# Kernel tuning notes

Measured on AMD Instinct MI355X. Metric: run time of the kernel, lower is better.

The kernel has to match this reference:

```python
import jax, jax.numpy as jnp
import numpy as np

NEG = -1000.0  # fill value for unmatched (type_mask != ti) entries

B, N, R = 4, 48, 16
T = 2 * R + 1          # 33 transition channels
Nc, L = 80, 3          # chains, chain length
Nt, Ni = 16, 5         # triples, chains per triple (uniform c_sections)


def setup_inputs() -> dict:
    key = jax.random.key(0)
    k1, k2, k3, k4, k5 = jax.random.split(key, 5)
    transitions = jax.random.normal(k1, (B, N, N, T), dtype=jnp.float32)
    type_mask = jax.random.randint(k2, (B, N, N, R), 0, 2, dtype=jnp.int32)
    rules = jax.random.randint(k3, (Nc, L), 0, T, dtype=jnp.int32)
    # stacked per-triple weights [Nt, Ni] (orig: ParameterList of [Ni,1]) and biases [Nt]
    weights = jax.random.normal(k4, (Nt, Ni), dtype=jnp.float32) / np.sqrt(Ni)
    biases = jax.random.uniform(k5, (Nt,), dtype=jnp.float32, minval=-1.0, maxval=1.0)
    return {"transitions": transitions, "type_mask": type_mask, "rules": rules,
            "weights": weights, "biases": biases}


def path_scores(transitions, rules):
    """Tropical (max-plus) chain DP.
    transitions: [B,N,N,T], rules: [Nc,L] -> scores [B,N,N,Nc]
    scores[b,x,y,c] = max over intermediate nodes of sum of hop scores.
    """
    Lc = rules.shape[1]
    hops = [transitions[..., rules[:, l]] for l in range(Lc)]  # each [B,N,N,Nc]
    # max-plus "matmul": s[b,x,y,c] = max_k hops0[b,x,k,c] + hops1[b,k,y,c]
    s = jnp.max(hops[0][:, :, :, None, :] + hops[1][:, None, :, :, :], axis=2)
    for l in range(2, Lc):
        s = jnp.max(s[:, :, :, None, :] + hops[l][:, None, :, :, :], axis=2)
    return s


def reference(transitions, type_mask, rules, weights, biases):
    # scores over all chains, exponentiated: [B,N,N,Nc]
    s = jnp.exp(path_scores(transitions, rules))
    # group chains by triple (uniform sections): [B,N,N,Nt,Ni]
    s = s.reshape(s.shape[0], s.shape[1], s.shape[2], Nt, Ni)
    # per-triple weighted sum + bias; one triple per relation so Nt == R
    comb = jnp.einsum('bxytc,tc->bxyt', s, weights) + biases  # [B,N,N,R]
    # masked_scatter: write score where type_mask[...,i] == ti (== 0 here), else -1000
    out = jnp.where(type_mask == 0, comb, NEG)
    return out
```

## Files before the change

kernel.cpp:

```cpp
#include <hip/hip_runtime.h>
#include <cmath>

#define BB 4
#define NN 48
#define PP (NN * NN)
#define TT 33
#define RR 16
#define NC 80
#define NI 5
#define NEG (-1000.0f)

#define XH 24
#define RS 52

__global__ __launch_bounds__(256) void transpose_kernel(
    const float* __restrict__ trans,
    float*       __restrict__ tpose)
{
    __shared__ float tile[64 * TT];
    const int blk = blockIdx.x;
    const int b   = blk / 36;
    const int p0  = (blk - b * 36) * 64;

    const float4* src = (const float4*)(trans + ((size_t)b * PP + p0) * TT);
    for (int j = threadIdx.x; j < 64 * TT / 4; j += 256)
        ((float4*)tile)[j] = src[j];
    __syncthreads();

    for (int j = threadIdx.x; j < TT * 64; j += 256) {
        const int t  = j >> 6;
        const int pl = j & 63;
        tpose[((size_t)b * TT + t) * PP + p0 + pl] = tile[pl * TT + t];
    }
}

__global__ __launch_bounds__(192) void chain_dp_kernel(
    const float* __restrict__ tpose,
    const int*   __restrict__ rules,
    const float* __restrict__ weights,
    float*       __restrict__ sw)
{
    __shared__ float H0R[XH * RS];
    __shared__ float H1 [PP];
    __shared__ float H2 [PP];
    __shared__ float S1R[XH * RS];

    const int blk = blockIdx.x;
    const int bc  = blk >> 1;
    const int xh  = blk & 1;
    const int b   = bc / NC;
    const int c   = bc - b * NC;
    const int x0r = xh * XH;

    const int r0 = rules[c * 3 + 0];
    const int r1 = rules[c * 3 + 1];
    const int r2 = rules[c * 3 + 2];

    const float* p0 = tpose + ((size_t)b * TT + r0) * PP + (size_t)x0r * NN;
    const float* p1 = tpose + ((size_t)b * TT + r1) * PP;
    const float* p2 = tpose + ((size_t)b * TT + r2) * PP;

    for (int j = threadIdx.x; j < PP / 4; j += 192) {
        ((float4*)H1)[j] = ((const float4*)p1)[j];
        ((float4*)H2)[j] = ((const float4*)p2)[j];
    }
    for (int j = threadIdx.x; j < XH * NN / 4; j += 192) {
        const int row = j / 12;
        const int cw  = j - row * 12;
        *(float4*)&H0R[row * RS + cw * 4] = ((const float4*)p0)[j];
    }
    __syncthreads();

    const int yt = threadIdx.x % 24;
    const int xt = threadIdx.x / 24;
    const int x0 = xt * 3;
    const int y0 = yt * 2;

    float acc[3][2];
    #pragma unroll
    for (int jx = 0; jx < 3; ++jx) { acc[jx][0] = -INFINITY; acc[jx][1] = -INFINITY; }

    #pragma unroll 4
    for (int k4 = 0; k4 < NN; k4 += 4) {
        const float4 a0 = *(const float4*)&H0R[(x0 + 0) * RS + k4];
        const float4 a1 = *(const float4*)&H0R[(x0 + 1) * RS + k4];
        const float4 a2 = *(const float4*)&H0R[(x0 + 2) * RS + k4];
        const float2 b0 = *(const float2*)&H1[(k4 + 0) * NN + y0];
        const float2 b1 = *(const float2*)&H1[(k4 + 1) * NN + y0];
        const float2 b2 = *(const float2*)&H1[(k4 + 2) * NN + y0];
        const float2 b3 = *(const float2*)&H1[(k4 + 3) * NN + y0];
        const float av[3][4] = {{a0.x, a0.y, a0.z, a0.w},
                                {a1.x, a1.y, a1.z, a1.w},
                                {a2.x, a2.y, a2.z, a2.w}};
        const float bv[4][2] = {{b0.x, b0.y}, {b1.x, b1.y},
                                {b2.x, b2.y}, {b3.x, b3.y}};
        #pragma unroll
        for (int jx = 0; jx < 3; ++jx)
            #pragma unroll
            for (int jy = 0; jy < 2; ++jy) {
                const float s0 = av[jx][0] + bv[0][jy];
                const float s1 = av[jx][1] + bv[1][jy];
                const float s2 = av[jx][2] + bv[2][jy];
                const float s3 = av[jx][3] + bv[3][jy];
                acc[jx][jy] = fmaxf(acc[jx][jy], fmaxf(s0, s1));
                acc[jx][jy] = fmaxf(acc[jx][jy], fmaxf(s2, s3));
            }
    }

    #pragma unroll
    for (int jx = 0; jx < 3; ++jx) {
        float2 v; v.x = acc[jx][0]; v.y = acc[jx][1];
        *(float2*)&S1R[(x0 + jx) * RS + y0] = v;
    }
    __syncthreads();

    float acc2[3][2];
    #pragma unroll
    for (int jx = 0; jx < 3; ++jx) { acc2[jx][0] = -INFINITY; acc2[jx][1] = -INFINITY; }

    #pragma unroll 4
    for (int k4 = 0; k4 < NN; k4 += 4) {
        const float4 a0 = *(const float4*)&S1R[(x0 + 0) * RS + k4];
        const float4 a1 = *(const float4*)&S1R[(x0 + 1) * RS + k4];
        const float4 a2 = *(const float4*)&S1R[(x0 + 2) * RS + k4];
        const float2 b0 = *(const float2*)&H2[(k4 + 0) * NN + y0];
        const float2 b1 = *(const float2*)&H2[(k4 + 1) * NN + y0];
        const float2 b2 = *(const float2*)&H2[(k4 + 2) * NN + y0];
        const float2 b3 = *(const float2*)&H2[(k4 + 3) * NN + y0];
        const float av[3][4] = {{a0.x, a0.y, a0.z, a0.w},
                                {a1.x, a1.y, a1.z, a1.w},
                                {a2.x, a2.y, a2.z, a2.w}};
        const float bv[4][2] = {{b0.x, b0.y}, {b1.x, b1.y},
                                {b2.x, b2.y}, {b3.x, b3.y}};
        #pragma unroll
        for (int jx = 0; jx < 3; ++jx)
            #pragma unroll
            for (int jy = 0; jy < 2; ++jy) {
                const float s0 = av[jx][0] + bv[0][jy];
                const float s1 = av[jx][1] + bv[1][jy];
                const float s2 = av[jx][2] + bv[2][jy];
                const float s3 = av[jx][3] + bv[3][jy];
                acc2[jx][jy] = fmaxf(acc2[jx][jy], fmaxf(s0, s1));
                acc2[jx][jy] = fmaxf(acc2[jx][jy], fmaxf(s2, s3));
            }
    }

    const float wgt = weights[c];
    float* outp = sw + (size_t)bc * PP + (size_t)x0r * NN;
    #pragma unroll
    for (int jx = 0; jx < 3; ++jx) {
        float2 o;
        o.x = __expf(acc2[jx][0]) * wgt;
        o.y = __expf(acc2[jx][1]) * wgt;
        *(float2*)&outp[(x0 + jx) * NN + y0] = o;
    }
}

__global__ __launch_bounds__(256) void combine_kernel(
    const float* __restrict__ sw,
    const int*   __restrict__ mask,
    const float* __restrict__ biases,
    float*       __restrict__ out)
{
    const int tq = threadIdx.x >> 7;
    const int pl = blockIdx.x * 128 + (threadIdx.x & 127);
    if (pl >= BB * PP) return;
    const int b = pl / PP;
    const int p = pl - b * PP;

    const float* base = sw + (size_t)b * NC * PP + p;

    float acc[8];
    #pragma unroll
    for (int tt = 0; tt < 8; ++tt) {
        const int t = tq * 8 + tt;
        float s = biases[t];
        #pragma unroll
        for (int i = 0; i < NI; ++i)
            s += base[(size_t)(t * NI + i) * PP];
        acc[tt] = s;
    }

    const int4* m4 = (const int4*)(mask + (size_t)pl * RR + tq * 8);
    float4*     o4 = (float4*)(out + (size_t)pl * RR + tq * 8);
    #pragma unroll
    for (int q = 0; q < 2; ++q) {
        const int4 m = m4[q];
        float4 o;
        o.x = (m.x == 0) ? acc[q * 4 + 0] : NEG;
        o.y = (m.y == 0) ? acc[q * 4 + 1] : NEG;
        o.z = (m.z == 0) ? acc[q * 4 + 2] : NEG;
        o.w = (m.w == 0) ? acc[q * 4 + 3] : NEG;
        o4[q] = o;
    }
}

extern "C" void kernel_launch(void* const* d_in, const int* in_sizes, int n_in,
                              void* d_out, int out_size, void* d_ws, size_t ws_size,
                              hipStream_t stream)
{
    const float* trans   = (const float*)d_in[0];
    const int*   mask    = (const int*)  d_in[1];
    const int*   rules   = (const int*)  d_in[2];
    const float* weights = (const float*)d_in[3];
    const float* biases  = (const float*)d_in[4];
    float* out = (float*)d_out;

    float* tpose = (float*)d_ws;
    float* sw    = tpose + (size_t)BB * TT * PP;

    transpose_kernel<<<BB * 36, 256, 0, stream>>>(trans, tpose);

    chain_dp_kernel<<<BB * NC * 2, 192, 0, stream>>>(tpose, rules, weights, sw);

    const int total2 = BB * PP * 2;
    combine_kernel<<<(total2 + 255) / 256, 256, 0, stream>>>(sw, mask, biases, out);
}
```

Baseline: 75.04 us.

## Process full 48x48 tile per block instead of splitting rows across two blocks

Each block of the chain DP kernel now computes all 48 rows for one (batch, chain) pair instead of half. This avoids loading H1 and H2 twice, once per half-block, and each thread's micro-tile grows from 3x2 to 3x4 with float4 B-operand loads. The grid is halved to 320 blocks, which may reduce occupancy and parallelism across CUs. Shared memory per block also rises because the H0R and S1R buffers double.

New measurement: 75.22 us. No clear change (+0.2%).

```diff
diff --git a/kernel.cpp b/kernel.cpp
--- a/kernel.cpp
+++ b/kernel.cpp
@@ -10,7 +10,6 @@
 #define NI 5
 #define NEG (-1000.0f)
 
-#define XH 24
 #define RS 52
 
 __global__ __launch_bounds__(256) void transpose_kernel(
@@ -40,64 +39,64 @@
     const float* __restrict__ weights,
     float*       __restrict__ sw)
 {
-    __shared__ float H0R[XH * RS];
+    __shared__ float H0R[NN * RS];
     __shared__ float H1 [PP];
     __shared__ float H2 [PP];
-    __shared__ float S1R[XH * RS];
-
-    const int blk = blockIdx.x;
-    const int bc  = blk >> 1;
-    const int xh  = blk & 1;
-    const int b   = bc / NC;
-    const int c   = bc - b * NC;
-    const int x0r = xh * XH;
+    __shared__ float S1R[NN * RS];
+
+    const int bc = blockIdx.x;
+    const int b  = bc / NC;
+    const int c  = bc - b * NC;
 
     const int r0 = rules[c * 3 + 0];
     const int r1 = rules[c * 3 + 1];
     const int r2 = rules[c * 3 + 2];
 
-    const float* p0 = tpose + ((size_t)b * TT + r0) * PP + (size_t)x0r * NN;
+    const float* p0 = tpose + ((size_t)b * TT + r0) * PP;
     const float* p1 = tpose + ((size_t)b * TT + r1) * PP;
     const float* p2 = tpose + ((size_t)b * TT + r2) * PP;
 
+    #pragma unroll
     for (int j = threadIdx.x; j < PP / 4; j += 192) {
         ((float4*)H1)[j] = ((const float4*)p1)[j];
         ((float4*)H2)[j] = ((const float4*)p2)[j];
-    }
-    for (int j = threadIdx.x; j < XH * NN / 4; j += 192) {
         const int row = j / 12;
         const int cw  = j - row * 12;
         *(float4*)&H0R[row * RS + cw * 4] = ((const float4*)p0)[j];
     }
     __syncthreads();
 
-    const int yt = threadIdx.x % 24;
-    const int xt = threadIdx.x / 24;
+    const int yt = threadIdx.x % 12;
+    const int xt = threadIdx.x / 12;
     const int x0 = xt * 3;
-    const int y0 = yt * 2;
-
-    float acc[3][2];
-    #pragma unroll
-    for (int jx = 0; jx < 3; ++jx) { acc[jx][0] = -INFINITY; acc[jx][1] = -INFINITY; }
+    const int y0 = yt * 4;
+
+    float acc[3][4];
+    #pragma unroll
+    for (int jx = 0; jx < 3; ++jx)
+        #pragma unroll
+        for (int jy = 0; jy < 4; ++jy) acc[jx][jy] = -INFINITY;
 
     #pragma unroll 4
     for (int k4 = 0; k4 < NN; k4 += 4) {
         const float4 a0 = *(const float4*)&H0R[(x0 + 0) * RS + k4];
         const float4 a1 = *(const float4*)&H0R[(x0 + 1) * RS + k4];
         const float4 a2 = *(const float4*)&H0R[(x0 + 2) * RS + k4];
-        const float2 b0 = *(const float2*)&H1[(k4 + 0) * NN + y0];
-        const float2 b1 = *(const float2*)&H1[(k4 + 1) * NN + y0];
-        const float2 b2 = *(const float2*)&H1[(k4 + 2) * NN + y0];
-        const float2 b3 = *(const float2*)&H1[(k4 + 3) * NN + y0];
+        const float4 b0 = *(const float4*)&H1[(k4 + 0) * NN + y0];
+        const float4 b1 = *(const float4*)&H1[(k4 + 1) * NN + y0];
+        const float4 b2 = *(const float4*)&H1[(k4 + 2) * NN + y0];
+        const float4 b3 = *(const float4*)&H1[(k4 + 3) * NN + y0];
         const float av[3][4] = {{a0.x, a0.y, a0.z, a0.w},
                                 {a1.x, a1.y, a1.z, a1.w},
                                 {a2.x, a2.y, a2.z, a2.w}};
-        const float bv[4][2] = {{b0.x, b0.y}, {b1.x, b1.y},
-                                {b2.x, b2.y}, {b3.x, b3.y}};
+        const float bv[4][4] = {{b0.x, b0.y, b0.z, b0.w},
+                                {b1.x, b1.y, b1.z, b1.w},
+                                {b2.x, b2.y, b2.z, b2.w},
+                                {b3.x, b3.y, b3.z, b3.w}};
         #pragma unroll
         for (int jx = 0; jx < 3; ++jx)
             #pragma unroll
-            for (int jy = 0; jy < 2; ++jy) {
+            for (int jy = 0; jy < 4; ++jy) {
                 const float s0 = av[jx][0] + bv[0][jy];
                 const float s1 = av[jx][1] + bv[1][jy];
                 const float s2 = av[jx][2] + bv[2][jy];
@@ -109,33 +108,38 @@
 
     #pragma unroll
     for (int jx = 0; jx < 3; ++jx) {
-        float2 v; v.x = acc[jx][0]; v.y = acc[jx][1];
-        *(float2*)&S1R[(x0 + jx) * RS + y0] = v;
+        float4 v;
+        v.x = acc[jx][0]; v.y = acc[jx][1]; v.z = acc[jx][2]; v.w = acc[jx][3];
+        *(float4*)&S1R[(x0 + jx) * RS + y0] = v;
     }
     __syncthreads();
 
-    float acc2[3][2];
-    #pragma unroll
-    for (int jx = 0; jx < 3; ++jx) { acc2[jx][0] = -INFINITY; acc2[jx][1] = -INFINITY; }
+    float acc2[3][4];
+    #pragma unroll
+    for (int jx = 0; jx < 3; ++jx)
+        #pragma unroll
+        for (int jy = 0; jy < 4; ++jy) acc2[jx][jy] = -INFINITY;
 
     #pragma unroll 4
     for (int k4 = 0; k4 < NN; k4 += 4) {
         const float4 a0 = *(const float4*)&S1R[(x0 + 0) * RS + k4];
         const float4 a1 = *(const float4*)&S1R[(x0 + 1) * RS + k4];
         const float4 a2 = *(const float4*)&S1R[(x0 + 2) * RS + k4];
-        const float2 b0 = *(const float2*)&H2[(k4 + 0) * NN + y0];
-        const float2 b1 = *(const float2*)&H2[(k4 + 1) * NN + y0];
-        const float2 b2 = *(const float2*)&H2[(k4 + 2) * NN + y0];
-        const float2 b3 = *(const float2*)&H2[(k4 + 3) * NN + y0];
+        const float4 b0 = *(const float4*)&H2[(k4 + 0) * NN + y0];
+        const float4 b1 = *(const float4*)&H2[(k4 + 1) * NN + y0];
+        const float4 b2 = *(const float4*)&H2[(k4 + 2) * NN + y0];
+        const float4 b3 = *(const float4*)&H2[(k4 + 3) * NN + y0];
         const float av[3][4] = {{a0.x, a0.y, a0.z, a0.w},
                                 {a1.x, a1.y, a1.z, a1.w},
                                 {a2.x, a2.y, a2.z, a2.w}};
-        const float bv[4][2] = {{b0.x, b0.y}, {b1.x, b1.y},
-                                {b2.x, b2.y}, {b3.x, b3.y}};
+        const float bv[4][4] = {{b0.x, b0.y, b0.z, b0.w},
+                                {b1.x, b1.y, b1.z, b1.w},
+                                {b2.x, b2.y, b2.z, b2.w},
+                                {b3.x, b3.y, b3.z, b3.w}};
         #pragma unroll
         for (int jx = 0; jx < 3; ++jx)
             #pragma unroll
-            for (int jy = 0; jy < 2; ++jy) {
+            for (int jy = 0; jy < 4; ++jy) {
                 const float s0 = av[jx][0] + bv[0][jy];
                 const float s1 = av[jx][1] + bv[1][jy];
                 const float s2 = av[jx][2] + bv[2][jy];
@@ -146,13 +150,15 @@
     }
 
     const float wgt = weights[c];
-    float* outp = sw + (size_t)bc * PP + (size_t)x0r * NN;
+    float* outp = sw + (size_t)bc * PP;
     #pragma unroll
     for (int jx = 0; jx < 3; ++jx) {
-        float2 o;
+        float4 o;
         o.x = __expf(acc2[jx][0]) * wgt;
         o.y = __expf(acc2[jx][1]) * wgt;
-        *(float2*)&outp[(x0 + jx) * NN + y0] = o;
+        o.z = __expf(acc2[jx][2]) * wgt;
+        o.w = __expf(acc2[jx][3]) * wgt;
+        *(float4*)&outp[(x0 + jx) * NN + y0] = o;
     }
 }
 
@@ -211,7 +217,7 @@
 
     transpose_kernel<<<BB * 36, 256, 0, stream>>>(trans, tpose);
 
-    chain_dp_kernel<<<BB * NC * 2, 192, 0, stream>>>(tpose, rules, weights, sw);
+    chain_dp_kernel<<<BB * NC, 192, 0, stream>>>(tpose, rules, weights, sw);
 
     const int total2 = BB * PP * 2;
     combine_kernel<<<(total2 + 255) / 256, 256, 0, stream>>>(sw, mask, biases, out);
```
